# Kernel tuning notes

Hardware: AMD Instinct MI355X
Metric: run time of the kernel (lower is better)

## Reference

```python
import jax, jax.numpy as jnp
import numpy as np

H = 5          # N_LSTM_nodes
NK = 32        # N_kernels
ND = 128       # N_dense_nodes
GH, GW = 20, 22


def _lstm_dir(x, Wih, Whh, b, reverse):
    # x: (P, in_dim); PyTorch gate order i, f, g, o; unbatched sequence of length P
    pre = x @ Wih.T + b  # (P, 4H) input contribution precomputed
    def step(carry, pt):
        h, c = carry
        g = pt + h @ Whh.T
        i, f, gg, o = jnp.split(g, 4)
        c = jax.nn.sigmoid(f) * c + jax.nn.sigmoid(i) * jnp.tanh(gg)
        h = jax.nn.sigmoid(o) * jnp.tanh(c)
        return (h, c), h
    z = jnp.zeros((H,), x.dtype)
    _, hs = jax.lax.scan(step, (z, z), pre, reverse=reverse)
    return hs  # (P, H), aligned with input order


def _bilstm(x, Wih, Whh, b):
    return jnp.concatenate([_lstm_dir(x, Wih[0], Whh[0], b[0], False),
                            _lstm_dir(x, Wih[1], Whh[1], b[1], True)], axis=-1)


def _conv(x, w, b, pad):
    y = jax.lax.conv_general_dilated(x, w, (1, 1), pad,
                                     dimension_numbers=('NCHW', 'OIHW', 'NCHW'))
    return y + b[None, :, None, None]


def _dense(x, w, b):
    return x @ w.T + b


def reference(Traces, Pstart, l0_Wih, l0_Whh, l0_b, l12_Wih, l12_Whh, l12_b,
              cw0, cb0, cw1, cb1, cw2, cb2, cw3, cb3,
              D1_w, D1_b, D2_w, D2_b, D3_w, D3_b,
              X1_w, X1_b, X2_w, X2_b, X3_w, X3_b,
              E1_w, E1_b, E2_w, E2_b, E3_w, E3_b,
              Xs, Ys, EventIndices, NEvents):
    lrelu, relu = jax.nn.leaky_relu, jax.nn.relu
    # 3-layer bidirectional LSTM over the concatenated pixel sequence
    x = _bilstm(Traces, l0_Wih, l0_Whh, l0_b)
    for l in range(2):
        x = _bilstm(x, l12_Wih[l], l12_Whh[l], l12_b[l])
    feat = x[:, 0]                                  # (P,)  LSTM_out[:, 0]
    P = feat.shape[0]
    # scatter: channels 0..H-1 get the LSTM feature, channel H gets Pstart
    vals = jnp.concatenate([jnp.broadcast_to(feat[:, None], (P, H)),
                            Pstart[:, None]], axis=1)          # (P, H+1)
    ch = jnp.arange(H + 1)
    Main = jnp.zeros((NEvents, H + 1, GH, GW), Traces.dtype)
    Main = Main.at[EventIndices[:, None], ch[None, :],
                   Xs[:, None], Ys[:, None]].set(vals)
    Main = jnp.where(jnp.isnan(Main), jnp.asarray(-1.0, Main.dtype), Main)
    Main = lrelu(_conv(Main, cw0, cb0, [(1, 1), (0, 0)]))  # (N, NK, 20, 20)
    Main = lrelu(_conv(Main, cw1, cb1, [(1, 1), (1, 1)]))
    Main = lrelu(_conv(Main, cw2, cb2, [(1, 1), (1, 1)]))
    Main = lrelu(_conv(Main, cw3, cb3, [(1, 1), (1, 1)]))
    Main = Main.reshape(NEvents, -1)                        # (N, NK*20*20)
    Main = relu(_dense(Main, D1_w, D1_b))
    Main = relu(_dense(Main, D2_w, D2_b))
    Main = relu(_dense(Main, D3_w, D3_b))
    Xm = relu(_dense(Main, X1_w, X1_b))
    Xm = relu(_dense(Xm, X2_w, X2_b))
    Xm = _dense(Xm, X3_w, X3_b)
    En = relu(_dense(Main, E1_w, E1_b))
    En = relu(_dense(En, E2_w, E2_b))
    En = _dense(En, E3_w, E3_b)
    out_w = jnp.ones((2,), Main.dtype)  # OutWeights = [1, 1]
    return jnp.concatenate([Xm, En], axis=1) * out_w


def setup_inputs() -> dict:
    key = jax.random.key(0)
    ks = jax.random.split(key, 40)
    P, N = 65536, 4096
    g = lambda i, shape, sc=0.1: jax.random.normal(ks[i], shape, jnp.float32) * sc
    return dict(
        Traces=jax.random.normal(ks[0], (P, 40), jnp.float32),
        Pstart=jax.random.uniform(ks[1], (P,), jnp.float32),
        l0_Wih=g(2, (2, 4 * H, 40)), l0_Whh=g(3, (2, 4 * H, H)), l0_b=g(4, (2, 4 * H)),
        l12_Wih=g(5, (2, 2, 4 * H, 2 * H)), l12_Whh=g(6, (2, 2, 4 * H, H)), l12_b=g(7, (2, 2, 4 * H)),
        cw0=g(8, (NK, H + 1, 3, 3)), cb0=g(9, (NK,)),
        cw1=g(10, (NK, NK, 3, 3)), cb1=g(11, (NK,)),
        cw2=g(12, (NK, NK, 3, 3)), cb2=g(13, (NK,)),
        cw3=g(14, (NK, NK, 3, 3)), cb3=g(15, (NK,)),
        D1_w=g(16, (ND, NK * 20 * 20), 0.01), D1_b=g(17, (ND,)),
        D2_w=g(18, (ND, ND)), D2_b=g(19, (ND,)),
        D3_w=g(20, (ND, ND)), D3_b=g(21, (ND,)),
        X1_w=g(22, (ND, ND)), X1_b=g(23, (ND,)),
        X2_w=g(24, (ND // 2, ND)), X2_b=g(25, (ND // 2,)),
        X3_w=g(26, (1, ND // 2)), X3_b=g(27, (1,)),
        E1_w=g(28, (ND, ND)), E1_b=g(29, (ND,)),
        E2_w=g(30, (ND // 2, ND)), E2_b=g(31, (ND // 2,)),
        E3_w=g(32, (1, ND // 2)), E3_b=g(33, (1,)),
        Xs=jax.random.randint(ks[34], (P,), 0, GH, jnp.int32),
        Ys=jax.random.randint(ks[35], (P,), 0, GW, jnp.int32),
        EventIndices=jnp.sort(jax.random.randint(ks[36], (P,), 0, N, jnp.int32)),
        NEvents=N,
    )
```

## Files before the change

kernel.cpp:

```cpp
#include <hip/hip_runtime.h>
#include <hip/hip_fp16.h>
#include <cstdint>
#include <cstddef>

#define PN 65536
#define NEV 4096
#define LCHUNK 4
#define LHALO 40
#define NCHUNK (PN / LCHUNK)
#define PRS 24

typedef _Float16 half8 __attribute__((ext_vector_type(8)));
typedef _Float16 half4 __attribute__((ext_vector_type(4)));
typedef float    f32x4 __attribute__((ext_vector_type(4)));
typedef float    f32x16 __attribute__((ext_vector_type(16)));

__device__ __forceinline__ float rcpf(float x)  { return __builtin_amdgcn_rcpf(x); }
__device__ __forceinline__ float sigf(float x)  { return rcpf(1.0f + __expf(-x)); }
__device__ __forceinline__ float tanh_(float x) { return 1.0f - 2.0f * rcpf(1.0f + __expf(2.0f * x)); }
__device__ __forceinline__ float lrelu(float x) { return x > 0.0f ? x : 0.01f * x; }


__global__ __launch_bounds__(64, 1) void k_scanA(
    const _Float16* __restrict__ pre, const float* __restrict__ whh,
    const float* __restrict__ wihn, const float* __restrict__ bn,
    float* __restrict__ po) {
  __shared__ float hsv[64][4][5];
  int tid = blockIdx.x * 64 + threadIdx.x;
  int d = tid / NCHUNK, c = tid - d * NCHUNK;
  float W[20][5];
  {
    const float4* wd4 = (const float4*)(whh + d * 100);
    float4 wv[25];
    #pragma unroll
    for (int i = 0; i < 25; ++i) wv[i] = wd4[i];
    float* wf = (float*)wv;
    #pragma unroll
    for (int j = 0; j < 20; ++j)
      #pragma unroll
      for (int k = 0; k < 5; ++k) W[j][k] = wf[j * 5 + k];
  }
  const _Float16* pd = pre + (size_t)d * PN * PRS;
  float h[5] = {0, 0, 0, 0, 0}, cs[5] = {0, 0, 0, 0, 0};
  int base = c * LCHUNK;
  int p, step, nsteps;
  if (d == 0) {
    int ps = base - LHALO; if (ps < 0) ps = 0;
    p = ps; step = 1; nsteps = base + LCHUNK - ps;
  } else {
    int ps = base + LCHUNK - 1 + LHALO; if (ps > PN - 1) ps = PN - 1;
    p = ps; step = -1; nsteps = ps - base + 1;
  }

  auto ld = [&](int pp, half8& A, half8& B, half4& C) {
    int pl = pp; if (pl < 0) pl = 0; if (pl >= PN) pl = PN - 1;
    const _Float16* rp = pd + (size_t)pl * PRS;
    A = *(const half8*)rp; B = *(const half8*)(rp + 8); C = *(const half4*)(rp + 16);
  };

  auto STEP = [&](half8 ca, half8 cb, half4 cc) {
    float g[20];
    #pragma unroll
    for (int i = 0; i < 8; ++i) { g[i] = (float)ca[i]; g[8 + i] = (float)cb[i]; }
    #pragma unroll
    for (int i = 0; i < 4; ++i) g[16 + i] = (float)cc[i];
    #pragma unroll
    for (int j = 0; j < 20; ++j) {
      #pragma unroll
      for (int k = 0; k < 5; ++k) g[j] = fmaf(W[j][k], h[k], g[j]);
    }
    #pragma unroll
    for (int k = 0; k < 5; ++k) {
      float it = sigf(g[k]);
      float ft = sigf(g[5 + k]);
      float gt = tanh_(g[10 + k]);
      float ot = sigf(g[15 + k]);
      cs[k] = fmaf(ft, cs[k], it * gt);
      h[k]  = ot * tanh_(cs[k]);
    }
    unsigned u = (unsigned)(p - base);
    if (u < (unsigned)LCHUNK) {
      #pragma unroll
      for (int k = 0; k < 5; ++k) hsv[threadIdx.x][u][k] = h[k];
    }
    p += step;
  };

  half8 a0, a1, a2, a3, b0, b1, b2, b3;
  half4 c0, c1, c2, c3;
  ld(p,            a0, b0, c0);
  ld(p + step,     a1, b1, c1);
  ld(p + 2 * step, a2, b2, c2);
  ld(p + 3 * step, a3, b3, c3);

  for (int s = 0; s < nsteps; s += 4) {
    half8 na0, na1, na2, na3, nb0, nb1, nb2, nb3;
    half4 nc0, nc1, nc2, nc3;
    ld(p + 4 * step, na0, nb0, nc0);
    ld(p + 5 * step, na1, nb1, nc1);
    ld(p + 6 * step, na2, nb2, nc2);
    ld(p + 7 * step, na3, nb3, nc3);
    STEP(a0, b0, c0);
    STEP(a1, b1, c1);
    STEP(a2, b2, c2);
    STEP(a3, b3, c3);
    a0 = na0; b0 = nb0; c0 = nc0;
    a1 = na1; b1 = nb1; c1 = nc1;
    a2 = na2; b2 = nb2; c2 = nc2;
    a3 = na3; b3 = nb3; c3 = nc3;
  }

  float Wp[40][5];
  #pragma unroll
  for (int j = 0; j < 40; ++j) {
    int addr = ((j >= 20) ? (200 + (j - 20) * 10) : (j * 10)) + d * 5;
    #pragma unroll
    for (int k = 0; k < 5; ++k) Wp[j][k] = wihn[addr + k];
  }
  #pragma unroll
  for (int oi = 0; oi < 4; ++oi) {
    float hv[5];
    #pragma unroll
    for (int k = 0; k < 5; ++k) hv[k] = hsv[threadIdx.x][oi][k];
    float pr[40];
    #pragma unroll
    for (int j = 0; j < 40; ++j) {
      float a = (d == 0) ? bn[j] : 0.0f;
      #pragma unroll
      for (int k = 0; k < 5; ++k) a = fmaf(Wp[j][k], hv[k], a);
      pr[j] = a;
    }
    float* dst = po + (size_t)(base + oi) * 80 + d * 40;
    #pragma unroll
    for (int q = 0; q < 10; ++q) {
      float4 v; v.x = pr[q * 4]; v.y = pr[q * 4 + 1]; v.z = pr[q * 4 + 2]; v.w = pr[q * 4 + 3];
      *(float4*)&dst[q * 4] = v;
    }
  }
}

__global__ __launch_bounds__(64, 1) void k_scanB(
    const float* __restrict__ pre32, const float* __restrict__ whh,
    const float* __restrict__ wihn, const float* __restrict__ bn,
    float* __restrict__ po, float* __restrict__ feat, int ndir, int rstride) {
  __shared__ float hsv[64][4][5];
  int tid = blockIdx.x * 64 + threadIdx.x;
  if (tid >= ndir * NCHUNK) return;
  int d = tid / NCHUNK, c = tid - d * NCHUNK;
  int soff = rstride >> 1;
  float W[20][5];
  {
    const float4* wd4 = (const float4*)(whh + d * 100);
    float4 wv[25];
    #pragma unroll
    for (int i = 0; i < 25; ++i) wv[i] = wd4[i];
    float* wf = (float*)wv;
    #pragma unroll
    for (int j = 0; j < 20; ++j)
      #pragma unroll
      for (int k = 0; k < 5; ++k) W[j][k] = wf[j * 5 + k];
  }
  float h[5] = {0, 0, 0, 0, 0}, cs[5] = {0, 0, 0, 0, 0};
  int base = c * LCHUNK;
  int p, step, nsteps;
  if (d == 0) {
    int ps = base - LHALO; if (ps < 0) ps = 0;
    p = ps; step = 1; nsteps = base + LCHUNK - ps;
  } else {
    int ps = base + LCHUNK - 1 + LHALO; if (ps > PN - 1) ps = PN - 1;
    p = ps; step = -1; nsteps = ps - base + 1;
  }

  auto ld32 = [&](int pp, f32x4* S) {
    int pl = pp; if (pl < 0) pl = 0; if (pl >= PN) pl = PN - 1;
    const float* r0 = pre32 + (size_t)pl * rstride + d * 20;
    const float* r1 = r0 + soff;
    #pragma unroll
    for (int q = 0; q < 5; ++q) S[q] = *(const f32x4*)&r0[q * 4];
    #pragma unroll
    for (int q = 0; q < 5; ++q) S[5 + q] = *(const f32x4*)&r1[q * 4];
  };

  auto STEP = [&](const f32x4* S) {
    float g[20];
    #pragma unroll
    for (int j = 0; j < 20; ++j) g[j] = S[j >> 2][j & 3] + S[5 + (j >> 2)][j & 3];
    #pragma unroll
    for (int j = 0; j < 20; ++j) {
      #pragma unroll
      for (int k = 0; k < 5; ++k) g[j] = fmaf(W[j][k], h[k], g[j]);
    }
    #pragma unroll
    for (int k = 0; k < 5; ++k) {
      float it = sigf(g[k]);
      float ft = sigf(g[5 + k]);
      float gt = tanh_(g[10 + k]);
      float ot = sigf(g[15 + k]);
      cs[k] = fmaf(ft, cs[k], it * gt);
      h[k]  = ot * tanh_(cs[k]);
    }
    unsigned u = (unsigned)(p - base);
    if (u < (unsigned)LCHUNK) {
      if (feat) {
        feat[p] = h[0];
      } else {
        #pragma unroll
        for (int k = 0; k < 5; ++k) hsv[threadIdx.x][u][k] = h[k];
      }
    }
    p += step;
  };

  f32x4 S0[10], S1[10];
  ld32(p, S0);
  for (int s = 0; s < nsteps; s += 2) {
    ld32(p + step, S1);
    STEP(S0);
    ld32(p + step, S0);
    STEP(S1);
  }

  if (!feat) {
    float Wp[20][5];
    #pragma unroll
    for (int j = 0; j < 20; ++j)
      #pragma unroll
      for (int k = 0; k < 5; ++k) Wp[j][k] = wihn[j * 10 + d * 5 + k];
    #pragma unroll
    for (int oi = 0; oi < 4; ++oi) {
      float hv[5];
      #pragma unroll
      for (int k = 0; k < 5; ++k) hv[k] = hsv[threadIdx.x][oi][k];
      float pr[20];
      #pragma unroll
      for (int j = 0; j < 20; ++j) {
        float a = (d == 0) ? bn[j] : 0.0f;
        #pragma unroll
        for (int k = 0; k < 5; ++k) a = fmaf(Wp[j][k], hv[k], a);
        pr[j] = a;
      }
      float* dst = po + (size_t)(base + oi) * 40 + d * 20;
      #pragma unroll
      for (int q = 0; q < 5; ++q) {
        float4 v; v.x = pr[q * 4]; v.y = pr[q * 4 + 1]; v.z = pr[q * 4 + 2]; v.w = pr[q * 4 + 3];
        *(float4*)&dst[q * 4] = v;
      }
    }
  }
}

__global__ void k_scat2(const int* __restrict__ ei, const int* __restrict__ xs,
                        const int* __restrict__ ys, const int* __restrict__ owner,
                        const float* __restrict__ feat, const float* __restrict__ pstart,
                        _Float16* __restrict__ main0g) {
  int p = blockIdx.x * 256 + threadIdx.x;
  if (p >= PN) return;
  int e = ei[p];
  int cell = e * 440 + xs[p] * 22 + ys[p];
  if (owner[cell] != p) return;
  _Float16 f = (_Float16)feat[p];
  _Float16* b = main0g + (size_t)cell * 8;
  #pragma unroll
  for (int ch = 0; ch < 5; ++ch) b[ch] = f;
  b[5] = (_Float16)pstart[p];
}

#define PREP_F ((2 * PN * 20) / 256)
#define PREP_A ((NEV * 440 * 4) / 256)
#define PREP_G (PN / 256)
#define PREP_C 144
#define PREP_D (128 * 13)
#define PREP_E 320
__global__ __launch_bounds__(256) void k_prep(
    const float* __restrict__ tr, const float* __restrict__ l0_Wih,
    const float* __restrict__ l0_b, _Float16* __restrict__ pre,
    _Float16* __restrict__ main0g, int* __restrict__ owner,
    const int* __restrict__ ei, const int* __restrict__ xs, const int* __restrict__ ys,
    const float* __restrict__ cw0, const float* __restrict__ cw1,
    const float* __restrict__ cw2, const float* __restrict__ cw3,
    _Float16* __restrict__ wt,
    const float* __restrict__ D1w, _Float16* __restrict__ d1wt,
    const float* __restrict__ D2, const float* __restrict__ D3,
    const float* __restrict__ X1, const float* __restrict__ X2,
    const float* __restrict__ E1, const float* __restrict__ E2,
    _Float16* __restrict__ mlpw) {
  __shared__ float t[32][33];
  int b = blockIdx.x;
  if (b < PREP_F) {
    int tid = b * 256 + threadIdx.x;
    int j = tid % 20;
    int p = (tid / 20) % PN;
    int d = tid / (20 * PN);
    const float4* t4 = (const float4*)(tr + (size_t)p * 40);
    const float4* w4 = (const float4*)(l0_Wih + (size_t)(d * 20 + j) * 40);
    float acc = l0_b[d * 20 + j];
    #pragma unroll
    for (int k = 0; k < 10; ++k) {
      float4 a = t4[k], w = w4[k];
      acc = fmaf(a.x, w.x, fmaf(a.y, w.y, fmaf(a.z, w.z, fmaf(a.w, w.w, acc))));
    }
    pre[((size_t)d * PN + p) * PRS + j] = (_Float16)acc;
  } else if (b < PREP_F + PREP_A) {
    int i = (b - PREP_F) * 256 + threadIdx.x;
    ((uint32_t*)main0g)[i] = 0u;
  } else if (b < PREP_F + PREP_A + PREP_G) {
    int p = (b - PREP_F - PREP_A) * 256 + threadIdx.x;
    int cell = ei[p] * 440 + xs[p] * 22 + ys[p];
    atomicMax(&owner[cell], p);
  } else if (b < PREP_F + PREP_A + PREP_G + PREP_C) {
    int tid = (b - PREP_F - PREP_A - PREP_G) * 256 + threadIdx.x;
    if (tid < 4 * 9216) {
      int L = tid / 9216, r = tid % 9216;
      int ic = r & 31, oc = (r >> 5) & 31, kykx = r >> 10;
      const float* w = (L == 0) ? cw0 : (L == 1) ? cw1 : (L == 2) ? cw2 : cw3;
      int Cin = (L == 0) ? 6 : 32;
      float v = (ic < Cin) ? w[(oc * Cin + ic) * 9 + kykx] : 0.0f;
      wt[tid] = (_Float16)v;
    }
  } else if (b < PREP_F + PREP_A + PREP_G + PREP_C + PREP_D) {
    int j = b - PREP_F - PREP_A - PREP_G - PREP_C;
    int od = j / 13;
    int p0 = (j % 13) * 32;
    int tx = threadIdx.x & 31, ty = threadIdx.x >> 5;
    for (int oc = ty; oc < 32; oc += 8) {
      int pix = p0 + tx;
      t[oc][tx] = (pix < 400) ? D1w[(size_t)od * 12800 + oc * 400 + pix] : 0.0f;
    }
    __syncthreads();
    for (int pp = ty; pp < 32; pp += 8) {
      int pix = p0 + pp;
      if (pix < 400) d1wt[(size_t)od * 12800 + pix * 32 + tx] = (_Float16)t[tx][pp];
    }
  } else {
    int i = (b - PREP_F - PREP_A - PREP_G - PREP_C - PREP_D) * 256 + threadIdx.x;
    if (i < 81920) {
      const float* s; int off;
      if      (i < 16384) { s = D2; off = 0; }
      else if (i < 32768) { s = D3; off = 16384; }
      else if (i < 49152) { s = X1; off = 32768; }
      else if (i < 57344) { s = X2; off = 49152; }
      else if (i < 73728) { s = E1; off = 57344; }
      else                { s = E2; off = 73728; }
      mlpw[i] = (_Float16)s[i - off];
    }
  }
}

#define ARS 22
#define ACT_N (22 * ARS * 40)
__global__ __launch_bounds__(256, 2) void k_conv(
    const _Float16* __restrict__ main0g, const _Float16* __restrict__ wtall,
    const float* __restrict__ cb0, const float* __restrict__ cb1,
    const float* __restrict__ cb2, const float* __restrict__ cb3,
    _Float16* __restrict__ gbuf) {
  __shared__ _Float16 lds[ACT_N];
  int e   = blockIdx.x;
  int tid = threadIdx.x;
  int lane = tid & 63, wv = tid >> 6;
  int ln = lane & 31, s = lane >> 5;

  const uint4* src = (const uint4*)(main0g + (size_t)e * 440 * 8);
  uint4 sv0, sv1;
  int si0 = tid, si1 = tid + 256;
  if (si0 < 440) sv0 = src[si0];
  if (si1 < 440) sv1 = src[si1];

  for (int i = tid; i < 176; i += 256) {
    int row = (i >= 88) ? 21 : 0;
    int j = (i >= 88) ? i - 88 : i;
    int col = j >> 2, hb = (j & 3) * 8;
    *(uint4*)&lds[(row * ARS + col) * 40 + hb] = (uint4){0, 0, 0, 0};
  }
  for (int i = tid; i < 1320; i += 256) {
    int row = 1 + i / 66;
    int j = i % 66;
    int col = j / 3, hb = 8 + (j % 3) * 8;
    *(uint4*)&lds[(row * ARS + col) * 40 + hb] = (uint4){0, 0, 0, 0};
  }
  if (si0 < 440) {
    int r = si0 / 22, c = si0 - r * 22;
    *(uint4*)&lds[((r + 1) * ARS + c) * 40] = sv0;
  }
  if (si1 < 440) {
    int r = si1 / 22, c = si1 - r * 22;
    *(uint4*)&lds[((r + 1) * ARS + c) * 40] = sv1;
  }
  int pix[4]; bool val[4];
  #pragma unroll
  for (int t = 0; t < 4; ++t) {
    int tile = (t < 3) ? (wv + t * 4) : 12;
    int n = tile * 32 + ln;
    val[t] = (n < 400);
    if (n > 399) n = 399;
    int y = n / 20, x = n - y * 20;
    pix[t] = y * ARS + x;
  }
  __syncthreads();

  const float* cbs[4] = {cb0, cb1, cb2, cb3};
  #pragma unroll
  for (int L = 0; L < 4; ++L) {
    const float* cb = cbs[L];
    f32x16 acc[4];
    {
      f32x16 binit;
      #pragma unroll
      for (int g = 0; g < 4; ++g) {
        f32x4 bv = *(const f32x4*)&cb[g * 8 + s * 4];
        #pragma unroll
        for (int j = 0; j < 4; ++j) binit[g * 4 + j] = bv[j];
      }
      #pragma unroll
      for (int t = 0; t < 4; ++t) acc[t] = binit;
    }
    const _Float16* wL = wtall + (size_t)L * 9216;
    #pragma unroll
    for (int h = 0; h < 2; ++h) {
      half8 afr[9];
      #pragma unroll
      for (int tap = 0; tap < 9; ++tap)
        afr[tap] = *(const half8*)&wL[(tap * 32 + ln) * 32 + h * 16 + s * 8];
      #pragma unroll
      for (int t = 0; t < 3; ++t) {
        int base = pix[t] * 40 + h * 16 + s * 8;
        #pragma unroll
        for (int ky = 0; ky < 3; ++ky)
          #pragma unroll
          for (int kx = 0; kx < 3; ++kx) {
            half8 bfr = *(const half8*)&lds[base + (ky * ARS + kx) * 40];
            acc[t] = __builtin_amdgcn_mfma_f32_32x32x16_f16(afr[ky * 3 + kx], bfr, acc[t], 0, 0, 0);
          }
      }
      if (wv == 0) {
        int base = pix[3] * 40 + h * 16 + s * 8;
        #pragma unroll
        for (int ky = 0; ky < 3; ++ky)
          #pragma unroll
          for (int kx = 0; kx < 3; ++kx) {
            half8 bfr = *(const half8*)&lds[base + (ky * ARS + kx) * 40];
            acc[3] = __builtin_amdgcn_mfma_f32_32x32x16_f16(afr[ky * 3 + kx], bfr, acc[3], 0, 0, 0);
          }
      }
      __builtin_amdgcn_sched_barrier(0);
    }
    __syncthreads();
    if (L < 3) {
      #pragma unroll
      for (int t = 0; t < 3; ++t) {
        int wa = (pix[t] + ARS + 1) * 40 + s * 4;
        #pragma unroll
        for (int g = 0; g < 4; ++g) {
          half4 hv;
          #pragma unroll
          for (int j = 0; j < 4; ++j) hv[j] = (_Float16)lrelu(acc[t][g * 4 + j]);
          *(half4*)&lds[wa + g * 8] = hv;
        }
      }
      if (wv == 0 && val[3]) {
        int wa = (pix[3] + ARS + 1) * 40 + s * 4;
        #pragma unroll
        for (int g = 0; g < 4; ++g) {
          half4 hv;
          #pragma unroll
          for (int j = 0; j < 4; ++j) hv[j] = (_Float16)lrelu(acc[3][g * 4 + j]);
          *(half4*)&lds[wa + g * 8] = hv;
        }
      }
      if (L == 0) {
        for (int i = tid; i < 176; i += 256) {
          int r = i >> 3, j = i & 7;
          int c = (j < 4) ? 0 : 21;
          int hb = (j & 3) * 8;
          *(uint4*)&lds[(r * ARS + c) * 40 + hb] = (uint4){0, 0, 0, 0};
        }
      }
      __syncthreads();
    } else {
      #pragma unroll
      for (int t = 0; t < 3; ++t) {
        int n = (wv + t * 4) * 32 + ln;
        _Float16* gp = &gbuf[((size_t)e * 400 + n) * 32 + s * 4];
        #pragma unroll
        for (int g = 0; g < 4; ++g) {
          half4 hv;
          #pragma unroll
          for (int j = 0; j < 4; ++j) hv[j] = (_Float16)lrelu(acc[t][g * 4 + j]);
          *(half4*)&gp[g * 8] = hv;
        }
      }
      if (wv == 0 && val[3]) {
        int n = 384 + ln;
        _Float16* gp = &gbuf[((size_t)e * 400 + n) * 32 + s * 4];
        #pragma unroll
        for (int g = 0; g < 4; ++g) {
          half4 hv;
          #pragma unroll
          for (int j = 0; j < 4; ++j) hv[j] = (_Float16)lrelu(acc[3][g * 4 + j]);
          *(half4*)&gp[g * 8] = hv;
        }
      }
    }
  }
}

__global__ __launch_bounds__(256, 2) void k_d1gemm(const _Float16* __restrict__ A,
    const _Float16* __restrict__ W, float* __restrict__ part) {
  __shared__ _Float16 ldsA[128 * 40];
  __shared__ _Float16 ldsW[128 * 40];
  int e0 = blockIdx.x * 128;
  int k0 = blockIdx.y * 800;
  int tid = threadIdx.x, lane = tid & 63, w = tid >> 6;
  int m_ = lane & 15, q = lane >> 4;
  f32x4 acc[8][2];
  #pragma unroll
  for (int ot = 0; ot < 8; ++ot)
    #pragma unroll
    for (int et = 0; et < 2; ++et) acc[ot][et] = (f32x4){0.f, 0.f, 0.f, 0.f};

  for (int kk = 0; kk < 800; kk += 32) {
    for (int i = tid; i < 512; i += 256) {
      int r = i >> 2, s = i & 3;
      *(uint4*)&ldsA[r * 40 + s * 8] = *(const uint4*)&A[(size_t)(e0 + r) * 12800 + k0 + kk + s * 8];
    }
    for (int i = tid; i < 512; i += 256) {
      int r = i >> 2, s = i & 3;
      *(uint4*)&ldsW[r * 40 + s * 8] = *(const uint4*)&W[(size_t)r * 12800 + k0 + kk + s * 8];
    }
    __syncthreads();
    half8 bfr[2];
    #pragma unroll
    for (int et = 0; et < 2; ++et)
      bfr[et] = *(const half8*)&ldsA[((w * 2 + et) * 16 + m_) * 40 + q * 8];
    #pragma unroll
    for (int ot = 0; ot < 8; ++ot) {
      half8 afr = *(const half8*)&ldsW[(ot * 16 + m_) * 40 + q * 8];
      acc[ot][0] = __builtin_amdgcn_mfma_f32_16x16x32_f16(afr, bfr[0], acc[ot][0], 0, 0, 0);
      acc[ot][1] = __builtin_amdgcn_mfma_f32_16x16x32_f16(afr, bfr[1], acc[ot][1], 0, 0, 0);
    }
    __syncthreads();
  }
  #pragma unroll
  for (int ot = 0; ot < 8; ++ot)
    #pragma unroll
    for (int et = 0; et < 2; ++et) {
      int od = ot * 16 + q * 4;
      int ev = e0 + (w * 2 + et) * 16 + m_;
      *(f32x4*)&part[((size_t)blockIdx.y * NEV + ev) * 128 + od] = acc[ot][et];
    }
}

__global__ __launch_bounds__(256) void k_mlp(
    const float* __restrict__ part, const float* __restrict__ D1_b,
    const _Float16* __restrict__ mlpw,
    const float* __restrict__ D2_b, const float* __restrict__ D3_b,
    const float* __restrict__ X1_b, const float* __restrict__ X2_b,
    const float* __restrict__ X3_w, const float* __restrict__ X3_b,
    const float* __restrict__ E1_b, const float* __restrict__ E2_b,
    const float* __restrict__ E3_w, const float* __restrict__ E3_b,
    float* __restrict__ out) {
  __shared__ _Float16 ldsA[16 * 132];
  __shared__ _Float16 ldsB[16 * 132];
  __shared__ _Float16 ldsW[128 * 132];
  int e0 = blockIdx.x * 16;
  int tid = threadIdx.x, lane = tid & 63, w = tid >> 6;
  int m_ = lane & 15, q = lane >> 4;

  for (int i = tid; i < 2048; i += 256) {
    int ev = i >> 7, od = i & 127;
    float s = D1_b[od];
    #pragma unroll
    for (int sp = 0; sp < 16; ++sp)
      s += part[((size_t)sp * NEV + e0 + ev) * 128 + od];
    ldsA[ev * 132 + od] = (_Float16)fmaxf(s, 0.f);
  }

  auto layer = [&](const _Float16* In, _Float16* Out, int odc,
                   const _Float16* wsrc, const float* bias) {
    const uint4* ws = (const uint4*)wsrc;
    for (int i = tid; i < odc * 16; i += 256) {
      int row = i >> 4, seg = i & 15;
      *(uint4*)&ldsW[row * 132 + seg * 8] = ws[i];
    }
    __syncthreads();
    int tpw = odc >> 6;
    int ot0 = w * tpw;
    half8 bfr[4];
    #pragma unroll
    for (int ks = 0; ks < 4; ++ks)
      bfr[ks] = *(const half8*)&In[m_ * 132 + ks * 32 + q * 8];
    f32x4 acc[2];
    for (int ot = 0; ot < tpw; ++ot) {
      acc[ot] = *(const f32x4*)&bias[(ot0 + ot) * 16 + q * 4];
      #pragma unroll
      for (int ks = 0; ks < 4; ++ks) {
        half8 afr = *(const half8*)&ldsW[((ot0 + ot) * 16 + m_) * 132 + ks * 32 + q * 8];
        acc[ot] = __builtin_amdgcn_mfma_f32_16x16x32_f16(afr, bfr[ks], acc[ot], 0, 0, 0);
      }
    }
    __syncthreads();
    for (int ot = 0; ot < tpw; ++ot) {
      half4 hv;
      #pragma unroll
      for (int r = 0; r < 4; ++r) hv[r] = (_Float16)fmaxf(acc[ot][r], 0.f);
      *(half4*)&Out[m_ * 132 + (ot0 + ot) * 16 + q * 4] = hv;
    }
  };

  __syncthreads();
  layer(ldsA, ldsB, 128, mlpw,          D2_b);
  layer(ldsB, ldsA, 128, mlpw + 16384,  D3_b);
  layer(ldsA, ldsB, 128, mlpw + 32768,  X1_b);
  layer(ldsB, ldsB,  64, mlpw + 49152,  X2_b);
  __syncthreads();
  if (tid < 16) {
    float a = X3_b[0];
    for (int k = 0; k < 64; ++k) a = fmaf((float)ldsB[tid * 132 + k], X3_w[k], a);
    out[(size_t)(e0 + tid) * 2] = a;
  }
  layer(ldsA, ldsB, 128, mlpw + 57344,  E1_b);
  layer(ldsB, ldsB,  64, mlpw + 73728,  E2_b);
  __syncthreads();
  if (tid < 16) {
    float a = E3_b[0];
    for (int k = 0; k < 64; ++k) a = fmaf((float)ldsB[tid * 132 + k], E3_w[k], a);
    out[(size_t)(e0 + tid) * 2 + 1] = a;
  }
}

extern "C" void kernel_launch(void* const* d_in, const int* in_sizes, int n_in,
                              void* d_out, int out_size, void* d_ws, size_t ws_size,
                              hipStream_t stream) {
  const float* Traces  = (const float*)d_in[0];
  const float* Pstart  = (const float*)d_in[1];
  const float* l0_Wih  = (const float*)d_in[2];
  const float* l0_Whh  = (const float*)d_in[3];
  const float* l0_b    = (const float*)d_in[4];
  const float* l12_Wih = (const float*)d_in[5];
  const float* l12_Whh = (const float*)d_in[6];
  const float* l12_b   = (const float*)d_in[7];
  const float* cw0 = (const float*)d_in[8];   const float* cb0 = (const float*)d_in[9];
  const float* cw1 = (const float*)d_in[10];  const float* cb1 = (const float*)d_in[11];
  const float* cw2 = (const float*)d_in[12];  const float* cb2 = (const float*)d_in[13];
  const float* cw3 = (const float*)d_in[14];  const float* cb3 = (const float*)d_in[15];
  const float* D1_w = (const float*)d_in[16]; const float* D1_b = (const float*)d_in[17];
  const float* D2_w = (const float*)d_in[18]; const float* D2_b = (const float*)d_in[19];
  const float* D3_w = (const float*)d_in[20]; const float* D3_b = (const float*)d_in[21];
  const float* X1_w = (const float*)d_in[22]; const float* X1_b = (const float*)d_in[23];
  const float* X2_w = (const float*)d_in[24]; const float* X2_b = (const float*)d_in[25];
  const float* X3_w = (const float*)d_in[26]; const float* X3_b = (const float*)d_in[27];
  const float* E1_w = (const float*)d_in[28]; const float* E1_b = (const float*)d_in[29];
  const float* E2_w = (const float*)d_in[30]; const float* E2_b = (const float*)d_in[31];
  const float* E3_w = (const float*)d_in[32]; const float* E3_b = (const float*)d_in[33];
  const int* Xs = (const int*)d_in[34];
  const int* Ys = (const int*)d_in[35];
  const int* EI = (const int*)d_in[36];
  float* out = (float*)d_out;

  char* wp = (char*)d_ws;
  auto alloc = [&](size_t bytes) -> char* {
    char* p = wp; wp += (bytes + 255) & ~(size_t)255; return p;
  };
  _Float16*  pre    = (_Float16*)alloc(sizeof(_Float16) * 2 * (size_t)PN * PRS);
  float*     feat   = (float*)alloc(sizeof(float) * PN);
  int*       owner  = (int*)alloc(sizeof(int) * NEV * 440);
  _Float16*  main0g = (_Float16*)alloc(sizeof(_Float16) * (size_t)NEV * 440 * 8);
  _Float16*  gbuf   = (_Float16*)alloc(sizeof(_Float16) * (size_t)NEV * 12800);
  _Float16*  wtall  = (_Float16*)alloc(sizeof(_Float16) * 4 * 9216);
  _Float16*  d1wt   = (_Float16*)alloc(sizeof(_Float16) * 128 * 12800);
  _Float16*  mlpw   = (_Float16*)alloc(sizeof(_Float16) * 81920);
  float*     d1part = (float*)owner;
  float*     pre1   = (float*)gbuf;
  float*     pre2   = (float*)gbuf + (size_t)PN * 80;

  k_prep<<<PREP_F + PREP_A + PREP_G + PREP_C + PREP_D + PREP_E, 256, 0, stream>>>(
      Traces, l0_Wih, l0_b, pre,
      main0g, owner, EI, Xs, Ys,
      cw0, cw1, cw2, cw3, wtall, D1_w, d1wt,
      D2_w, D3_w, X1_w, X2_w, E1_w, E2_w, mlpw);

  k_scanA<<<(2 * NCHUNK) / 64, 64, 0, stream>>>(pre, l0_Whh, l12_Wih, l12_b, pre1);
  k_scanB<<<(2 * NCHUNK) / 64, 64, 0, stream>>>(pre1, l12_Whh, l12_Wih + 400, l12_b + 40,
                                                pre2, nullptr, 2, 80);
  k_scanB<<<NCHUNK / 64, 64, 0, stream>>>(pre2, l12_Whh + 200, nullptr, nullptr,
                                          nullptr, feat, 1, 40);

  k_scat2<<<PN / 256, 256, 0, stream>>>(EI, Xs, Ys, owner, feat, Pstart, main0g);

  k_conv<<<NEV, 256, 0, stream>>>(main0g, wtall, cb0, cb1, cb2, cb3, gbuf);

  dim3 g1(32, 16);
  k_d1gemm<<<g1, 256, 0, stream>>>(gbuf, d1wt, d1part);
  k_mlp<<<NEV / 16, 256, 0, stream>>>(d1part, D1_b, mlpw, D2_b, D3_b, X1_b, X2_b, X3_w, X3_b,
                                      E1_b, E2_b, E3_w, E3_b, out);
}
```

Before: 476.3 us.

## Interleave two independent LSTM chunks per thread in scan kernels

Each thread in the chunked LSTM scan kernels now processes two adjacent chunks, interleaving their recurrence steps so that two independent dependency chains can overlap instruction latency. The loop count is fixed at halo plus chunk length, with a per-chunk start offset that skips steps before the sequence boundary, and the grid is halved. This trades fewer threads and waves, plus higher register pressure, for more instruction-level parallelism within each thread.

```diff
diff --git a/kernel.cpp b/kernel.cpp
--- a/kernel.cpp
+++ b/kernel.cpp
@@ -8,6 +8,8 @@
 #define LCHUNK 4
 #define LHALO 40
 #define NCHUNK (PN / LCHUNK)
+#define NHALF (NCHUNK / 2)
+#define NSTEPS (LHALO + LCHUNK)
 #define PRS 24
 
 typedef _Float16 half8 __attribute__((ext_vector_type(8)));
@@ -21,13 +23,24 @@
 __device__ __forceinline__ float lrelu(float x) { return x > 0.0f ? x : 0.01f * x; }
 
 
+struct Row16 { half8 a, b; half4 c; };
+struct Row32 { f32x4 s[10]; };
+
 __global__ __launch_bounds__(64, 1) void k_scanA(
     const _Float16* __restrict__ pre, const float* __restrict__ whh,
     const float* __restrict__ wihn, const float* __restrict__ bn,
     float* __restrict__ po) {
-  __shared__ float hsv[64][4][5];
+  __shared__ float hsv[64][2][4][5];
   int tid = blockIdx.x * 64 + threadIdx.x;
-  int d = tid / NCHUNK, c = tid - d * NCHUNK;
+  int d = tid / NHALF, ct = tid - d * NHALF;
+  int cA = 2 * ct, cB = 2 * ct + 1;
+  int baseA = cA * LCHUNK, baseB = cB * LCHUNK;
+  int sgn = (d == 0) ? 1 : -1;
+  int p0A = (d == 0) ? (baseA - LHALO) : (baseA + LCHUNK - 1 + LHALO);
+  int p0B = (d == 0) ? (baseB - LHALO) : (baseB + LCHUNK - 1 + LHALO);
+  int s0A = (d == 0) ? ((p0A < 0) ? -p0A : 0) : ((p0A > PN - 1) ? (p0A - (PN - 1)) : 0);
+  int s0B = (d == 0) ? ((p0B < 0) ? -p0B : 0) : ((p0B > PN - 1) ? (p0B - (PN - 1)) : 0);
+
   float W[20][5];
   {
     const float4* wd4 = (const float4*)(whh + d * 100);
@@ -41,29 +54,26 @@
       for (int k = 0; k < 5; ++k) W[j][k] = wf[j * 5 + k];
   }
   const _Float16* pd = pre + (size_t)d * PN * PRS;
-  float h[5] = {0, 0, 0, 0, 0}, cs[5] = {0, 0, 0, 0, 0};
-  int base = c * LCHUNK;
-  int p, step, nsteps;
-  if (d == 0) {
-    int ps = base - LHALO; if (ps < 0) ps = 0;
-    p = ps; step = 1; nsteps = base + LCHUNK - ps;
-  } else {
-    int ps = base + LCHUNK - 1 + LHALO; if (ps > PN - 1) ps = PN - 1;
-    p = ps; step = -1; nsteps = ps - base + 1;
-  }
-
-  auto ld = [&](int pp, half8& A, half8& B, half4& C) {
-    int pl = pp; if (pl < 0) pl = 0; if (pl >= PN) pl = PN - 1;
+  float hA[5] = {0, 0, 0, 0, 0}, csA[5] = {0, 0, 0, 0, 0};
+  float hB[5] = {0, 0, 0, 0, 0}, csB[5] = {0, 0, 0, 0, 0};
+
+  auto ld = [&](int p0, int s) -> Row16 {
+    int pl = p0 + sgn * s;
+    if (pl < 0) pl = 0; if (pl >= PN) pl = PN - 1;
     const _Float16* rp = pd + (size_t)pl * PRS;
-    A = *(const half8*)rp; B = *(const half8*)(rp + 8); C = *(const half4*)(rp + 16);
+    Row16 r;
+    r.a = *(const half8*)rp; r.b = *(const half8*)(rp + 8); r.c = *(const half4*)(rp + 16);
+    return r;
   };
 
-  auto STEP = [&](half8 ca, half8 cb, half4 cc) {
+  auto STEP = [&](float* h, float* cs, Row16 r, int p0, int base, int s, int s0, int slot) {
+    if (s < s0) return;
+    int p = p0 + sgn * s;
     float g[20];
     #pragma unroll
-    for (int i = 0; i < 8; ++i) { g[i] = (float)ca[i]; g[8 + i] = (float)cb[i]; }
-    #pragma unroll
-    for (int i = 0; i < 4; ++i) g[16 + i] = (float)cc[i];
+    for (int i = 0; i < 8; ++i) { g[i] = (float)r.a[i]; g[8 + i] = (float)r.b[i]; }
+    #pragma unroll
+    for (int i = 0; i < 4; ++i) g[16 + i] = (float)r.c[i];
     #pragma unroll
     for (int j = 0; j < 20; ++j) {
       #pragma unroll
@@ -81,33 +91,20 @@
     unsigned u = (unsigned)(p - base);
     if (u < (unsigned)LCHUNK) {
       #pragma unroll
-      for (int k = 0; k < 5; ++k) hsv[threadIdx.x][u][k] = h[k];
-    }
-    p += step;
+      for (int k = 0; k < 5; ++k) hsv[threadIdx.x][slot][u][k] = h[k];
+    }
   };
 
-  half8 a0, a1, a2, a3, b0, b1, b2, b3;
-  half4 c0, c1, c2, c3;
-  ld(p,            a0, b0, c0);
-  ld(p + step,     a1, b1, c1);
-  ld(p + 2 * step, a2, b2, c2);
-  ld(p + 3 * step, a3, b3, c3);
-
-  for (int s = 0; s < nsteps; s += 4) {
-    half8 na0, na1, na2, na3, nb0, nb1, nb2, nb3;
-    half4 nc0, nc1, nc2, nc3;
-    ld(p + 4 * step, na0, nb0, nc0);
-    ld(p + 5 * step, na1, nb1, nc1);
-    ld(p + 6 * step, na2, nb2, nc2);
-    ld(p + 7 * step, na3, nb3, nc3);
-    STEP(a0, b0, c0);
-    STEP(a1, b1, c1);
-    STEP(a2, b2, c2);
-    STEP(a3, b3, c3);
-    a0 = na0; b0 = nb0; c0 = nc0;
-    a1 = na1; b1 = nb1; c1 = nc1;
-    a2 = na2; b2 = nb2; c2 = nc2;
-    a3 = na3; b3 = nb3; c3 = nc3;
+  Row16 rA0 = ld(p0A, 0), rA1 = ld(p0A, 1);
+  Row16 rB0 = ld(p0B, 0), rB1 = ld(p0B, 1);
+  for (int s = 0; s < NSTEPS; s += 2) {
+    Row16 nA0 = ld(p0A, s + 2), nA1 = ld(p0A, s + 3);
+    Row16 nB0 = ld(p0B, s + 2), nB1 = ld(p0B, s + 3);
+    STEP(hA, csA, rA0, p0A, baseA, s,     s0A, 0);
+    STEP(hB, csB, rB0, p0B, baseB, s,     s0B, 1);
+    STEP(hA, csA, rA1, p0A, baseA, s + 1, s0A, 0);
+    STEP(hB, csB, rB1, p0B, baseB, s + 1, s0B, 1);
+    rA0 = nA0; rA1 = nA1; rB0 = nB0; rB1 = nB1;
   }
 
   float Wp[40][5];
@@ -118,23 +115,27 @@
     for (int k = 0; k < 5; ++k) Wp[j][k] = wihn[addr + k];
   }
   #pragma unroll
-  for (int oi = 0; oi < 4; ++oi) {
-    float hv[5];
-    #pragma unroll
-    for (int k = 0; k < 5; ++k) hv[k] = hsv[threadIdx.x][oi][k];
-    float pr[40];
-    #pragma unroll
-    for (int j = 0; j < 40; ++j) {
-      float a = (d == 0) ? bn[j] : 0.0f;
-      #pragma unroll
-      for (int k = 0; k < 5; ++k) a = fmaf(Wp[j][k], hv[k], a);
-      pr[j] = a;
-    }
-    float* dst = po + (size_t)(base + oi) * 80 + d * 40;
-    #pragma unroll
-    for (int q = 0; q < 10; ++q) {
-      float4 v; v.x = pr[q * 4]; v.y = pr[q * 4 + 1]; v.z = pr[q * 4 + 2]; v.w = pr[q * 4 + 3];
-      *(float4*)&dst[q * 4] = v;
+  for (int X = 0; X < 2; ++X) {
+    int base = (X == 0) ? baseA : baseB;
+    #pragma unroll
+    for (int oi = 0; oi < 4; ++oi) {
+      float hv[5];
+      #pragma unroll
+      for (int k = 0; k < 5; ++k) hv[k] = hsv[threadIdx.x][X][oi][k];
+      float pr[40];
+      #pragma unroll
+      for (int j = 0; j < 40; ++j) {
+        float a = (d == 0) ? bn[j] : 0.0f;
+        #pragma unroll
+        for (int k = 0; k < 5; ++k) a = fmaf(Wp[j][k], hv[k], a);
+        pr[j] = a;
+      }
+      float* dst = po + (size_t)(base + oi) * 80 + d * 40;
+      #pragma unroll
+      for (int q = 0; q < 10; ++q) {
+        float4 v; v.x = pr[q * 4]; v.y = pr[q * 4 + 1]; v.z = pr[q * 4 + 2]; v.w = pr[q * 4 + 3];
+        *(float4*)&dst[q * 4] = v;
+      }
     }
   }
 }
@@ -143,11 +144,19 @@
     const float* __restrict__ pre32, const float* __restrict__ whh,
     const float* __restrict__ wihn, const float* __restrict__ bn,
     float* __restrict__ po, float* __restrict__ feat, int ndir, int rstride) {
-  __shared__ float hsv[64][4][5];
+  __shared__ float hsv[64][2][4][5];
   int tid = blockIdx.x * 64 + threadIdx.x;
-  if (tid >= ndir * NCHUNK) return;
-  int d = tid / NCHUNK, c = tid - d * NCHUNK;
+  if (tid >= ndir * NHALF) return;
+  int d = tid / NHALF, ct = tid - d * NHALF;
+  int cA = 2 * ct, cB = 2 * ct + 1;
+  int baseA = cA * LCHUNK, baseB = cB * LCHUNK;
+  int sgn = (d == 0) ? 1 : -1;
+  int p0A = (d == 0) ? (baseA - LHALO) : (baseA + LCHUNK - 1 + LHALO);
+  int p0B = (d == 0) ? (baseB - LHALO) : (baseB + LCHUNK - 1 + LHALO);
+  int s0A = (d == 0) ? ((p0A < 0) ? -p0A : 0) : ((p0A > PN - 1) ? (p0A - (PN - 1)) : 0);
+  int s0B = (d == 0) ? ((p0B < 0) ? -p0B : 0) : ((p0B > PN - 1) ? (p0B - (PN - 1)) : 0);
   int soff = rstride >> 1;
+
   float W[20][5];
   {
     const float4* wd4 = (const float4*)(whh + d * 100);
@@ -160,31 +169,28 @@
       #pragma unroll
       for (int k = 0; k < 5; ++k) W[j][k] = wf[j * 5 + k];
   }
-  float h[5] = {0, 0, 0, 0, 0}, cs[5] = {0, 0, 0, 0, 0};
-  int base = c * LCHUNK;
-  int p, step, nsteps;
-  if (d == 0) {
-    int ps = base - LHALO; if (ps < 0) ps = 0;
-    p = ps; step = 1; nsteps = base + LCHUNK - ps;
-  } else {
-    int ps = base + LCHUNK - 1 + LHALO; if (ps > PN - 1) ps = PN - 1;
-    p = ps; step = -1; nsteps = ps - base + 1;
-  }
-
-  auto ld32 = [&](int pp, f32x4* S) {
-    int pl = pp; if (pl < 0) pl = 0; if (pl >= PN) pl = PN - 1;
+  float hA[5] = {0, 0, 0, 0, 0}, csA[5] = {0, 0, 0, 0, 0};
+  float hB[5] = {0, 0, 0, 0, 0}, csB[5] = {0, 0, 0, 0, 0};
+
+  auto ld = [&](int p0, int s) -> Row32 {
+    int pl = p0 + sgn * s;
+    if (pl < 0) pl = 0; if (pl >= PN) pl = PN - 1;
     const float* r0 = pre32 + (size_t)pl * rstride + d * 20;
     const float* r1 = r0 + soff;
-    #pragma unroll
-    for (int q = 0; q < 5; ++q) S[q] = *(const f32x4*)&r0[q * 4];
-    #pragma unroll
-    for (int q = 0; q < 5; ++q) S[5 + q] = *(const f32x4*)&r1[q * 4];
+    Row32 r;
+    #pragma unroll
+    for (int q = 0; q < 5; ++q) r.s[q] = *(const f32x4*)&r0[q * 4];
+    #pragma unroll
+    for (int q = 0; q < 5; ++q) r.s[5 + q] = *(const f32x4*)&r1[q * 4];
+    return r;
   };
 
-  auto STEP = [&](const f32x4* S) {
+  auto STEP = [&](float* h, float* cs, const Row32& r, int p0, int base, int s, int s0, int slot) {
+    if (s < s0) return;
+    int p = p0 + sgn * s;
     float g[20];
     #pragma unroll
-    for (int j = 0; j < 20; ++j) g[j] = S[j >> 2][j & 3] + S[5 + (j >> 2)][j & 3];
+    for (int j = 0; j < 20; ++j) g[j] = r.s[j >> 2][j & 3] + r.s[5 + (j >> 2)][j & 3];
     #pragma unroll
     for (int j = 0; j < 20; ++j) {
       #pragma unroll
@@ -205,19 +211,19 @@
         feat[p] = h[0];
       } else {
         #pragma unroll
-        for (int k = 0; k < 5; ++k) hsv[threadIdx.x][u][k] = h[k];
-      }
-    }
-    p += step;
+        for (int k = 0; k < 5; ++k) hsv[threadIdx.x][slot][u][k] = h[k];
+      }
+    }
   };
 
-  f32x4 S0[10], S1[10];
-  ld32(p, S0);
-  for (int s = 0; s < nsteps; s += 2) {
-    ld32(p + step, S1);
-    STEP(S0);
-    ld32(p + step, S0);
-    STEP(S1);
+  Row32 rA0 = ld(p0A, 0), rB0 = ld(p0B, 0);
+  for (int s = 0; s < NSTEPS; s += 2) {
+    Row32 rA1 = ld(p0A, s + 1), rB1 = ld(p0B, s + 1);
+    STEP(hA, csA, rA0, p0A, baseA, s, s0A, 0);
+    STEP(hB, csB, rB0, p0B, baseB, s, s0B, 1);
+    rA0 = ld(p0A, s + 2); rB0 = ld(p0B, s + 2);
+    STEP(hA, csA, rA1, p0A, baseA, s + 1, s0A, 0);
+    STEP(hB, csB, rB1, p0B, baseB, s + 1, s0B, 1);
   }
 
   if (!feat) {
@@ -227,23 +233,27 @@
       #pragma unroll
       for (int k = 0; k < 5; ++k) Wp[j][k] = wihn[j * 10 + d * 5 + k];
     #pragma unroll
-    for (int oi = 0; oi < 4; ++oi) {
-      float hv[5];
-      #pragma unroll
-      for (int k = 0; k < 5; ++k) hv[k] = hsv[threadIdx.x][oi][k];
-      float pr[20];
-      #pragma unroll
-      for (int j = 0; j < 20; ++j) {
-        float a = (d == 0) ? bn[j] : 0.0f;
-        #pragma unroll
-        for (int k = 0; k < 5; ++k) a = fmaf(Wp[j][k], hv[k], a);
-        pr[j] = a;
-      }
-      float* dst = po + (size_t)(base + oi) * 40 + d * 20;
-      #pragma unroll
-      for (int q = 0; q < 5; ++q) {
-        float4 v; v.x = pr[q * 4]; v.y = pr[q * 4 + 1]; v.z = pr[q * 4 + 2]; v.w = pr[q * 4 + 3];
-        *(float4*)&dst[q * 4] = v;
+    for (int X = 0; X < 2; ++X) {
+      int base = (X == 0) ? baseA : baseB;
+      #pragma unroll
+      for (int oi = 0; oi < 4; ++oi) {
+        float hv[5];
+        #pragma unroll
+        for (int k = 0; k < 5; ++k) hv[k] = hsv[threadIdx.x][X][oi][k];
+        float pr[20];
+        #pragma unroll
+        for (int j = 0; j < 20; ++j) {
+          float a = (d == 0) ? bn[j] : 0.0f;
+          #pragma unroll
+          for (int k = 0; k < 5; ++k) a = fmaf(Wp[j][k], hv[k], a);
+          pr[j] = a;
+        }
+        float* dst = po + (size_t)(base + oi) * 40 + d * 20;
+        #pragma unroll
+        for (int q = 0; q < 5; ++q) {
+          float4 v; v.x = pr[q * 4]; v.y = pr[q * 4 + 1]; v.z = pr[q * 4 + 2]; v.w = pr[q * 4 + 3];
+          *(float4*)&dst[q * 4] = v;
+        }
       }
     }
   }
@@ -678,11 +688,11 @@
       cw0, cw1, cw2, cw3, wtall, D1_w, d1wt,
       D2_w, D3_w, X1_w, X2_w, E1_w, E2_w, mlpw);
 
-  k_scanA<<<(2 * NCHUNK) / 64, 64, 0, stream>>>(pre, l0_Whh, l12_Wih, l12_b, pre1);
-  k_scanB<<<(2 * NCHUNK) / 64, 64, 0, stream>>>(pre1, l12_Whh, l12_Wih + 400, l12_b + 40,
-                                                pre2, nullptr, 2, 80);
-  k_scanB<<<NCHUNK / 64, 64, 0, stream>>>(pre2, l12_Whh + 200, nullptr, nullptr,
-                                          nullptr, feat, 1, 40);
+  k_scanA<<<NCHUNK / 64, 64, 0, stream>>>(pre, l0_Whh, l12_Wih, l12_b, pre1);
+  k_scanB<<<NCHUNK / 64, 64, 0, stream>>>(pre1, l12_Whh, l12_Wih + 400, l12_b + 40,
+                                          pre2, nullptr, 2, 80);
+  k_scanB<<<NHALF / 64, 64, 0, stream>>>(pre2, l12_Whh + 200, nullptr, nullptr,
+                                         nullptr, feat, 1, 40);
 
   k_scat2<<<PN / 256, 256, 0, stream>>>(EI, Xs, Ys, owner, feat, Pstart, main0g);
 
```

Result: slower. 559.7 us (+17.5%).
